# Performance work log

Hardware: AMD Instinct MI355X
Metric: run time of the kernel (lower is better)

The kernel has to match this reference:

```python
import jax, jax.numpy as jnp
import numpy as np

N_NODES = 5000
N_EDGES = 50000
BATCH = 8
SEQ = 12
IN_CH = 2
HID = 64
OUT_CH = 1
K = 3
N_LAYERS = 2


def setup_inputs() -> dict:
    key = jax.random.key(0)
    ks = jax.random.split(key, 20)
    d = {}
    d["x"] = jax.random.normal(ks[0], (BATCH, SEQ, N_NODES, IN_CH), dtype=jnp.float32)
    d["edge_index"] = jax.random.randint(ks[1], (2, N_EDGES), 0, N_NODES, dtype=jnp.int32)

    def w(k, fin):
        return jax.random.normal(k, (2, K, fin, HID), dtype=jnp.float32) * 0.05

    fins = [IN_CH + HID, HID + HID]
    i = 2
    for l in range(N_LAYERS):
        for g in ("z", "r", "h"):
            d["W" + g + str(l)] = w(ks[i], fins[l]); i += 1
            d["b" + g + str(l)] = jnp.zeros((HID,), jnp.float32)
    d["Wo"] = jax.random.normal(ks[i], (HID, OUT_CH), dtype=jnp.float32) * 0.05
    d["bo"] = jnp.zeros((OUT_CH,), jnp.float32)
    return d


def reference(x, edge_index,
              Wz0, bz0, Wr0, br0, Wh0, bh0,
              Wz1, bz1, Wr1, br1, Wh1, bh1,
              Wo, bo):
    B, T, N, _ = x.shape
    src, dst = edge_index[0], edge_index[1]
    ones = jnp.ones(src.shape, x.dtype)
    deg_out = jax.ops.segment_sum(ones, src, num_segments=N)
    deg_in = jax.ops.segment_sum(ones, dst, num_segments=N)
    inv = lambda dgr: jnp.where(dgr > 0, 1.0 / dgr, 0.0)
    norm_out = inv(deg_out)[src]  # [E], 1/deg_out(src)
    norm_in = inv(deg_in)[dst]    # [E], 1/deg_in(dst)

    def prop(X, norm):
        # X: [N, B, F] -> sparse matvec via gather/scatter
        msg = norm[:, None, None] * X[src]
        return jax.ops.segment_sum(msg, dst, num_segments=N)

    def dconv(X, W, b):
        # X: [N, B, Fin]; W: [2, K, Fin, H]; dual-direction Chebyshev diffusion
        H = jnp.einsum('nbf,fh->nbh', X, W[0, 0] + W[1, 0])
        Tx0o = Tx0i = X
        Tx1o = prop(X, norm_out)
        Tx1i = prop(X, norm_in)
        H = H + jnp.einsum('nbf,fh->nbh', Tx1o, W[0, 1]) \
              + jnp.einsum('nbf,fh->nbh', Tx1i, W[1, 1])
        for k in range(2, W.shape[1]):
            Tx2o = 2.0 * prop(Tx1o, norm_out) - Tx0o
            Tx2i = 2.0 * prop(Tx1i, norm_in) - Tx0i
            H = H + jnp.einsum('nbf,fh->nbh', Tx2o, W[0, k]) \
                  + jnp.einsum('nbf,fh->nbh', Tx2i, W[1, k])
            Tx0o, Tx1o = Tx1o, Tx2o
            Tx0i, Tx1i = Tx1i, Tx2i
        return H + b

    def cell(Xin, H, p):
        Wz, bz, Wr, br, Wh, bh = p
        XH = jnp.concatenate([Xin, H], axis=-1)
        Z = jax.nn.sigmoid(dconv(XH, Wz, bz))
        R = jax.nn.sigmoid(dconv(XH, Wr, br))
        Ht = jnp.tanh(dconv(jnp.concatenate([Xin, H * R], axis=-1), Wh, bh))
        return Z * H + (1.0 - Z) * Ht

    layers = [(Wz0, bz0, Wr0, br0, Wh0, bh0), (Wz1, bz1, Wr1, br1, Wh1, bh1)]
    hid = Wo.shape[0]
    h0 = jnp.zeros((len(layers), N, B, hid), x.dtype)
    xs = jnp.transpose(x, (1, 2, 0, 3))  # [T, N, B, F]

    def step(h, xt):
        inp = xt
        new_h = []
        for l, p in enumerate(layers):
            hl = cell(inp, h[l], p)
            new_h.append(hl)
            inp = hl
        h = jnp.stack(new_h)
        out = jnp.einsum('nbh,ho->nbo', h[-1], Wo) + bo
        return h, out

    _, outs = jax.lax.scan(step, h0, xs)      # [T, N, B, O]
    return jnp.transpose(outs, (2, 0, 1, 3))  # [B, T, N, O]
```

## Files before the change

### kernel.cpp

```cpp
#include <hip/hip_runtime.h>
#include <math.h>

#define NNODES 5000
#define NEDGES 50000
#define SEQT 12
#define NB 40000
#define MAXDEG 128

typedef __attribute__((ext_vector_type(8))) _Float16 half8;
typedef __attribute__((ext_vector_type(2))) _Float16 half2v;
typedef __attribute__((ext_vector_type(4))) float f32x4;


__global__ void count_deg_k(const int* __restrict__ ei, int* deg_out, int* deg_in){
    int e = blockIdx.x*blockDim.x + threadIdx.x;
    if (e < NEDGES){
        atomicAdd(&deg_out[ei[e]], 1);
        atomicAdd(&deg_in[ei[NEDGES + e]], 1);
    }
}

__global__ void scan_k(const int* __restrict__ deg_in, int* __restrict__ row_ptr){
    __shared__ int part[256];
    int tid = threadIdx.x;
    int base = tid*20;
    int loc[20]; int s = 0;
    for (int i=0;i<20;i++){
        int idx = base+i;
        int v = (idx < NNODES) ? deg_in[idx] : 0;
        loc[i] = s; s += v;
    }
    part[tid] = s;
    __syncthreads();
    for (int off=1; off<256; off<<=1){
        int v = (tid>=off) ? part[tid-off] : 0;
        __syncthreads();
        part[tid] += v;
        __syncthreads();
    }
    int prev = (tid==0) ? 0 : part[tid-1];
    for (int i=0;i<20;i++){
        int idx = base+i;
        if (idx < NNODES) row_ptr[idx] = prev + loc[i];
    }
    if (tid==255) row_ptr[NNODES] = part[255];
}

__global__ void fill_csr_k(const int* __restrict__ ei, const int* __restrict__ deg_out,
                           const int* __restrict__ deg_in, const int* __restrict__ row_ptr,
                           int* cursor, int* __restrict__ csr_src,
                           float* __restrict__ csr_wo, float* __restrict__ csr_wi){
    int e = blockIdx.x*blockDim.x + threadIdx.x;
    if (e >= NEDGES) return;
    int s = ei[e], d = ei[NEDGES+e];
    int pos = atomicAdd(&cursor[d], 1);
    int slot = row_ptr[d] + pos;
    csr_src[slot] = s;
    csr_wo[slot] = 1.f/(float)deg_out[s];
    csr_wi[slot] = 1.f/(float)deg_in[d];
}

__global__ void prepack_x_k(const float* __restrict__ x, _Float16* __restrict__ Xtph){
    int idx = blockIdx.x*256 + threadIdx.x;
    if (idx >= SEQT*NB*2) return;
    int tt = idx / (NB*2);
    int r2 = idx - tt*(NB*2);
    int row = r2 >> 1, f = r2 & 1;
    int n = row >> 3, b = row & 7;
    Xtph[idx] = (_Float16)x[((size_t)(b*SEQT+tt)*NNODES + n)*2 + f];
}

__device__ __forceinline__ float wfetch(const float* __restrict__ W, int F, int slot, int f, int c){
    const float* p0 = W + ((size_t)0*F + f)*64 + c;
    const float* p1 = W + ((size_t)1*F + f)*64 + c;
    const float* p2 = W + ((size_t)2*F + f)*64 + c;
    const float* p3 = W + ((size_t)3*F + f)*64 + c;
    const float* p4 = W + ((size_t)4*F + f)*64 + c;
    const float* p5 = W + ((size_t)5*F + f)*64 + c;
    switch(slot){
        case 0: return *p0 + *p3 - *p2 - *p5;
        case 1: return *p1;
        case 2: return *p4;
        case 3: return 2.f * *p2;
        default: return 2.f * *p5;
    }
}

__global__ void pack_l0_k(const float* __restrict__ W, _Float16* __restrict__ wh){
    int idx = blockIdx.x*256 + threadIdx.x;
    if (idx >= 4*11*64) return;
    int lane = idx & 63, rest = idx >> 6;
    int ks = rest % 11, cf = rest / 11;
    int col = cf*16 + (lane & 15);
    int kb = ks*32 + ((lane>>4)<<3);
    size_t o = ((size_t)(ks*4 + cf)*64 + lane)*8;
    for (int j=0;j<8;j++){
        int k = kb + j;
        float v = 0.f;
        if (ks == 0){
            if (k < 10) v = wfetch(W, 66, k>>1, k&1, col);
        } else {
            int slot = (ks-1)>>1;
            int f = 2 + k - 32 - 64*slot;
            v = wfetch(W, 66, slot, f, col);
        }
        wh[o+j] = (_Float16)v;
    }
}

__global__ void pack_l1_k(const float* __restrict__ W, _Float16* __restrict__ wh){
    int idx = blockIdx.x*256 + threadIdx.x;
    if (idx >= 4*20*64) return;
    int lane = idx & 63, rest = idx >> 6;
    int ks = rest % 20, cf = rest / 20;
    int col = cf*16 + (lane & 15);
    int kb = ks*32 + ((lane>>4)<<3);
    int slot = ks >> 2;
    size_t o = ((size_t)(ks*4 + cf)*64 + lane)*8;
    for (int j=0;j<8;j++){
        int k = kb + j;
        int f = k - slot*128;
        wh[o+j] = (_Float16)wfetch(W, 128, slot, f, col);
    }
}


__global__ __launch_bounds__(64) void k_f1(int aCount,
    const _Float16* __restrict__ h0h, const _Float16* __restrict__ h1h,
    _Float16* __restrict__ T1o64, _Float16* __restrict__ T1i64,
    const _Float16* __restrict__ Xt,
    _Float16* __restrict__ Th1o, _Float16* __restrict__ Th1i, _Float16* __restrict__ XTh,
    const int* __restrict__ rp, const int* __restrict__ cs,
    const float* __restrict__ cwo, const float* __restrict__ cwi){
    __shared__ int s_o[MAXDEG]; __shared__ float swo[MAXDEG], swi[MAXDEG];
    const int bx = blockIdx.x;
    const bool isA = bx < aCount;
    const int n = isA ? bx : bx - aCount;
    int beg = rp[n], deg = rp[n+1]-beg;
    int nst = deg < MAXDEG ? deg : MAXDEG;
    for (int j=threadIdx.x; j<nst; j+=64){
        s_o[j] = cs[beg+j]*512;
        swo[j] = cwo[beg+j]; swi[j] = cwi[beg+j];
    }
    __syncthreads();
    const _Float16* S = isA ? h1h : h0h;
    _Float16* Yo = isA ? T1o64 : Th1o;
    _Float16* Yi = isA ? T1i64 : Th1i;
    int off = threadIdx.x*8;
    {
        float ao[8] = {0,0,0,0,0,0,0,0}, ai[8] = {0,0,0,0,0,0,0,0};
        for (int j=0;j<nst;j++){
            half8 v = *(const half8*)(S + s_o[j] + off);
            float wo=swo[j], wi=swi[j];
            #pragma unroll
            for (int e=0;e<8;e++){
                float xv = (float)v[e];
                ao[e]=fmaf(wo,xv,ao[e]); ai[e]=fmaf(wi,xv,ai[e]);
            }
        }
        for (int j=nst;j<deg;j++){
            half8 v = *(const half8*)(S + (size_t)cs[beg+j]*512 + off);
            float wo=cwo[beg+j], wi=cwi[beg+j];
            #pragma unroll
            for (int e=0;e<8;e++){
                float xv = (float)v[e];
                ao[e]=fmaf(wo,xv,ao[e]); ai[e]=fmaf(wi,xv,ai[e]);
            }
        }
        half8 po, pi;
        #pragma unroll
        for (int e=0;e<8;e++){ po[e]=(_Float16)ao[e]; pi[e]=(_Float16)ai[e]; }
        *(half8*)(Yo + (size_t)n*512 + off) = po;
        *(half8*)(Yi + (size_t)n*512 + off) = pi;
    }
    if (!isA && threadIdx.x < 8){
        int b = threadIdx.x;
        float ax0=0,ax1=0, ay0=0,ay1=0;
        for (int j=0;j<nst;j++){
            int src = s_o[j] >> 9;
            half2v v = *(const half2v*)(Xt + src*16 + b*2);
            float x0=(float)v[0], x1=(float)v[1];
            ax0=fmaf(swo[j],x0,ax0); ax1=fmaf(swo[j],x1,ax1);
            ay0=fmaf(swi[j],x0,ay0); ay1=fmaf(swi[j],x1,ay1);
        }
        for (int j=nst;j<deg;j++){
            int src = cs[beg+j];
            half2v v = *(const half2v*)(Xt + src*16 + b*2);
            float x0=(float)v[0], x1=(float)v[1];
            ax0=fmaf(cwo[beg+j],x0,ax0); ax1=fmaf(cwo[beg+j],x1,ax1);
            ay0=fmaf(cwi[beg+j],x0,ay0); ay1=fmaf(cwi[beg+j],x1,ay1);
        }
        size_t ro = (size_t)(n*8 + b)*32;
        XTh[ro+0] = Xt[(size_t)(n*8+b)*2+0];
        XTh[ro+1] = Xt[(size_t)(n*8+b)*2+1];
        XTh[ro+2] = (_Float16)ax0; XTh[ro+3] = (_Float16)ax1;
        XTh[ro+4] = (_Float16)ay0; XTh[ro+5] = (_Float16)ay1;
    }
}

__global__ __launch_bounds__(64) void k_f2(int aCount,
    const _Float16* __restrict__ T1o64, const _Float16* __restrict__ T1i64,
    _Float16* __restrict__ U2o64, _Float16* __restrict__ U2i64,
    const _Float16* __restrict__ Th1o, const _Float16* __restrict__ Th1i,
    _Float16* __restrict__ Th2o, _Float16* __restrict__ Th2i, _Float16* __restrict__ XTh,
    const int* __restrict__ rp, const int* __restrict__ cs,
    const float* __restrict__ cwo, const float* __restrict__ cwi){
    __shared__ int s_o[MAXDEG]; __shared__ float s_w[MAXDEG];
    const int bx = blockIdx.x;
    const bool isA = bx < aCount;
    const int idx = isA ? bx : bx - aCount;
    const int n = idx >> 1, sel = idx & 1;
    const float* cw = sel ? cwi : cwo;
    int beg = rp[n], deg = rp[n+1]-beg;
    int nst = deg < MAXDEG ? deg : MAXDEG;
    for (int j=threadIdx.x; j<nst; j+=64){
        s_o[j] = cs[beg+j]*512;
        s_w[j] = cw[beg+j];
    }
    __syncthreads();
    const _Float16* S = isA ? (sel ? T1i64 : T1o64) : (sel ? Th1i : Th1o);
    _Float16* U = isA ? (sel ? U2i64 : U2o64) : (sel ? Th2i : Th2o);
    int off = threadIdx.x*8;
    {
        float a[8] = {0,0,0,0,0,0,0,0};
        for (int j=0;j<nst;j++){
            half8 v = *(const half8*)(S + s_o[j] + off);
            float w=s_w[j];
            #pragma unroll
            for (int e=0;e<8;e++) a[e]=fmaf(w,(float)v[e],a[e]);
        }
        for (int j=nst;j<deg;j++){
            half8 v = *(const half8*)(S + (size_t)cs[beg+j]*512 + off);
            float w=cw[beg+j];
            #pragma unroll
            for (int e=0;e<8;e++) a[e]=fmaf(w,(float)v[e],a[e]);
        }
        half8 p;
        #pragma unroll
        for (int e=0;e<8;e++) p[e]=(_Float16)a[e];
        *(half8*)(U + (size_t)n*512 + off) = p;
    }
    if (!isA && threadIdx.x < 8){
        int b = threadIdx.x;
        int xo = 2 + 2*sel;
        float a0=0,a1=0;
        for (int j=0;j<nst;j++){
            int src = s_o[j] >> 9;
            half2v v = *(const half2v*)(XTh + (size_t)src*256 + b*32 + xo);
            a0=fmaf(s_w[j],(float)v[0],a0); a1=fmaf(s_w[j],(float)v[1],a1);
        }
        for (int j=nst;j<deg;j++){
            int src = cs[beg+j];
            float w = cw[beg+j];
            half2v v = *(const half2v*)(XTh + (size_t)src*256 + b*32 + xo);
            a0=fmaf(w,(float)v[0],a0); a1=fmaf(w,(float)v[1],a1);
        }
        size_t ro = (size_t)(n*8 + b)*32 + 6 + 2*sel;
        XTh[ro+0] = (_Float16)a0; XTh[ro+1] = (_Float16)a1;
    }
}

__global__ __launch_bounds__(64) void k_f4(int aCount,
    const _Float16* __restrict__ SA, _Float16* __restrict__ YoA, _Float16* __restrict__ YiA,
    const _Float16* __restrict__ SB, _Float16* __restrict__ YoB, _Float16* __restrict__ YiB,
    const int* __restrict__ rp, const int* __restrict__ cs,
    const float* __restrict__ cwo, const float* __restrict__ cwi){
    __shared__ int s_o[MAXDEG]; __shared__ float swo[MAXDEG], swi[MAXDEG];
    const int bx = blockIdx.x;
    const bool isA = bx < aCount;
    const int n = isA ? bx : bx - aCount;
    const _Float16* S = isA ? SA : SB;
    _Float16* Yo = isA ? YoA : YoB;
    _Float16* Yi = isA ? YiA : YiB;
    int beg = rp[n], deg = rp[n+1]-beg;
    int nst = deg < MAXDEG ? deg : MAXDEG;
    for (int j=threadIdx.x; j<nst; j+=64){
        s_o[j] = cs[beg+j]*512;
        swo[j] = cwo[beg+j]; swi[j] = cwi[beg+j];
    }
    __syncthreads();
    int off = threadIdx.x*8;
    float ao[8] = {0,0,0,0,0,0,0,0}, ai[8] = {0,0,0,0,0,0,0,0};
    for (int j=0;j<nst;j++){
        half8 v = *(const half8*)(S + s_o[j] + off);
        float wo=swo[j], wi=swi[j];
        #pragma unroll
        for (int e=0;e<8;e++){
            float xv = (float)v[e];
            ao[e]=fmaf(wo,xv,ao[e]); ai[e]=fmaf(wi,xv,ai[e]);
        }
    }
    for (int j=nst;j<deg;j++){
        half8 v = *(const half8*)(S + (size_t)cs[beg+j]*512 + off);
        float wo=cwo[beg+j], wi=cwi[beg+j];
        #pragma unroll
        for (int e=0;e<8;e++){
            float xv = (float)v[e];
            ao[e]=fmaf(wo,xv,ao[e]); ai[e]=fmaf(wi,xv,ai[e]);
        }
    }
    half8 po, pi;
    #pragma unroll
    for (int e=0;e<8;e++){ po[e]=(_Float16)ao[e]; pi[e]=(_Float16)ai[e]; }
    *(half8*)(Yo + (size_t)n*512 + off) = po;
    *(half8*)(Yi + (size_t)n*512 + off) = pi;
}

__global__ __launch_bounds__(64) void k_f5(int aCount,
    const _Float16* __restrict__ T1oA, const _Float16* __restrict__ T1iA,
    _Float16* __restrict__ U2oA, _Float16* __restrict__ U2iA,
    const _Float16* __restrict__ T1oB, const _Float16* __restrict__ T1iB,
    _Float16* __restrict__ U2oB, _Float16* __restrict__ U2iB,
    const int* __restrict__ rp, const int* __restrict__ cs,
    const float* __restrict__ cwo, const float* __restrict__ cwi){
    __shared__ int s_o[MAXDEG]; __shared__ float s_w[MAXDEG];
    const int bx = blockIdx.x;
    const bool isA = bx < aCount;
    const int idx = isA ? bx : bx - aCount;
    const int n = idx >> 1, sel = idx & 1;
    const _Float16* S = isA ? (sel ? T1iA : T1oA) : (sel ? T1iB : T1oB);
    _Float16* U = isA ? (sel ? U2iA : U2oA) : (sel ? U2iB : U2oB);
    const float* cw = sel ? cwi : cwo;
    int beg = rp[n], deg = rp[n+1]-beg;
    int nst = deg < MAXDEG ? deg : MAXDEG;
    for (int j=threadIdx.x; j<nst; j+=64){
        s_o[j] = cs[beg+j]*512;
        s_w[j] = cw[beg+j];
    }
    __syncthreads();
    int off = threadIdx.x*8;
    float a[8] = {0,0,0,0,0,0,0,0};
    for (int j=0;j<nst;j++){
        half8 v = *(const half8*)(S + s_o[j] + off);
        float w=s_w[j];
        #pragma unroll
        for (int e=0;e<8;e++) a[e]=fmaf(w,(float)v[e],a[e]);
    }
    for (int j=nst;j<deg;j++){
        half8 v = *(const half8*)(S + (size_t)cs[beg+j]*512 + off);
        float w=cw[beg+j];
        #pragma unroll
        for (int e=0;e<8;e++) a[e]=fmaf(w,(float)v[e],a[e]);
    }
    half8 p;
    #pragma unroll
    for (int e=0;e<8;e++) p[e]=(_Float16)a[e];
    *(half8*)(U + (size_t)n*512 + off) = p;
}


struct KD { const _Float16* a; int st; };
struct GA { KD kd[20]; };

template<int NK, int NG, int EPI>
__device__ __forceinline__ void gemm_body(char* smemraw, int bxm, const GA& ga,
    const _Float16* __restrict__ wh0, const float* __restrict__ b0,
    const _Float16* __restrict__ wh1, const float* __restrict__ b1,
    float* __restrict__ Z, _Float16* __restrict__ Gout,
    float* __restrict__ Hf, _Float16* __restrict__ Hh,
    const float* __restrict__ Wo, const float* __restrict__ bo,
    float* __restrict__ out, int t){
    _Float16* ldsb = (_Float16*)smemraw;
    float* spr = (float*)(smemraw + (size_t)4*NG*2048);
    const int tid = threadIdx.x;
    const int lane = tid & 63, wv = tid >> 6, rl = lane & 15, kg = lane >> 4;
    const int m0 = bxm*64 + (wv&1)*32;
    const int cfb = (wv>>1)*2;
    const _Float16* wsrc[2] = {wh0, wh1};

    half8 srg[NG];
    half8 a0, a1, a0n, a1n;

    auto sload = [&](int ks){
        #pragma unroll
        for (int j=0;j<NG;j++)
            srg[j] = *(const half8*)(wsrc[j] + (size_t)ks*2048 + tid*8);
    };
    auto swrite = [&](int buf){
        #pragma unroll
        for (int j=0;j<NG;j++)
            *(half8*)&ldsb[buf*(NG*2048) + j*2048 + tid*8] = srg[j];
    };
    auto aload = [&](int ks, half8& x0, half8& x1){
        const _Float16* base = ga.kd[ks].a;
        const int st = ga.kd[ks].st;
        x0 = *(const half8*)(base + (size_t)(m0+rl)*st + kg*8);
        x1 = *(const half8*)(base + (size_t)(m0+16+rl)*st + kg*8);
    };

    f32x4 acc[NG][2][2];
    #pragma unroll
    for (int g=0; g<NG; ++g)
        #pragma unroll
        for (int cc=0; cc<2; ++cc)
            #pragma unroll
            for (int mr=0; mr<2; ++mr){
                acc[g][cc][mr][0]=0.f; acc[g][cc][mr][1]=0.f;
                acc[g][cc][mr][2]=0.f; acc[g][cc][mr][3]=0.f;
            }

    sload(0); swrite(0);
    if (NK>1) sload(1);
    aload(0, a0, a1);
    __syncthreads();
    for (int ks=0; ks<NK; ++ks){
        const int cur = ks & 1;
        if (ks+1 < NK){ swrite(cur^1); aload(ks+1, a0n, a1n); }
        if (ks+2 < NK) sload(ks+2);
        #pragma unroll
        for (int g=0; g<NG; ++g){
            #pragma unroll
            for (int cc=0; cc<2; ++cc){
                half8 bv = *(const half8*)&ldsb[cur*(NG*2048) + g*2048 + (cfb+cc)*512 + lane*8];
                acc[g][cc][0] = __builtin_amdgcn_mfma_f32_16x16x32_f16(a0, bv, acc[g][cc][0], 0, 0, 0);
                acc[g][cc][1] = __builtin_amdgcn_mfma_f32_16x16x32_f16(a1, bv, acc[g][cc][1], 0, 0, 0);
            }
        }
        __syncthreads();
        a0 = a0n; a1 = a1n;
    }

    if constexpr (EPI == 0){
        #pragma unroll
        for (int cc=0; cc<2; ++cc){
            const int col = (cfb+cc)*16 + rl;
            float bzv = b0[col], brv = b1[col];
            #pragma unroll
            for (int mr=0; mr<2; ++mr)
                #pragma unroll
                for (int i=0;i<4;i++){
                    int row = m0 + mr*16 + kg*4 + i;
                    float z = 1.f/(1.f+__expf(-(acc[0][cc][mr][i] + bzv)));
                    float r = 1.f/(1.f+__expf(-(acc[NG-1][cc][mr][i] + brv)));
                    size_t ix = (size_t)row*64 + col;
                    Z[ix] = z;
                    Gout[ix] = (_Float16)(Hf[ix]*r);
                }
        }
    } else {
        float pr[2][4] = {{0.f,0.f,0.f,0.f},{0.f,0.f,0.f,0.f}};
        #pragma unroll
        for (int cc=0; cc<2; ++cc){
            const int col = (cfb+cc)*16 + rl;
            float bv = b0[col];
            float wo_c = 0.f;
            if constexpr (EPI == 2) wo_c = Wo[col];
            #pragma unroll
            for (int mr=0; mr<2; ++mr)
                #pragma unroll
                for (int i=0;i<4;i++){
                    int row = m0 + mr*16 + kg*4 + i;
                    float ht = tanhf(acc[0][cc][mr][i] + bv);
                    size_t ix = (size_t)row*64 + col;
                    float z = Z[ix];
                    float hn = z*Hf[ix] + (1.f-z)*ht;
                    Hf[ix] = hn;
                    Hh[ix] = (_Float16)hn;
                    if constexpr (EPI == 2) pr[mr][i] = fmaf(hn, wo_c, pr[mr][i]);
                }
        }
        if constexpr (EPI == 2){
            #pragma unroll
            for (int mr=0; mr<2; ++mr)
                #pragma unroll
                for (int i=0;i<4;i++){
                    float v = pr[mr][i];
                    v += __shfl_xor(v, 1);
                    v += __shfl_xor(v, 2);
                    v += __shfl_xor(v, 4);
                    v += __shfl_xor(v, 8);
                    if (rl == 0) spr[wv*32 + mr*16 + kg*4 + i] = v;
                }
            __syncthreads();
            if (tid < 64){
                int r = tid;
                float v = spr[(r>>5)*32 + (r&31)] + spr[((r>>5)|2)*32 + (r&31)] + bo[0];
                int row = bxm*64 + r;
                int n = row >> 3, b = row & 7;
                out[(size_t)(b*SEQT + t)*NNODES + n] = v;
            }
        }
    }
}

__global__ __launch_bounds__(256) void k_f3(int aCount,
    GA gaA, const _Float16* whA0, const float* bA0, const _Float16* whA1, const float* bA1,
    float* ZA, _Float16* GoA, float* HfA,
    GA gaB, const _Float16* whB0, const float* bB0, const _Float16* whB1, const float* bB1,
    float* ZB, _Float16* GoB, float* HfB){
    __shared__ __align__(16) char smem[4*2*2048 + 512];
    if (blockIdx.x < aCount)
        gemm_body<20,2,0>(smem, blockIdx.x, gaA, whA0, bA0, whA1, bA1,
                          ZA, GoA, HfA, nullptr, nullptr, nullptr, nullptr, 0);
    else
        gemm_body<11,2,0>(smem, blockIdx.x - aCount, gaB, whB0, bB0, whB1, bB1,
                          ZB, GoB, HfB, nullptr, nullptr, nullptr, nullptr, 0);
}

__global__ __launch_bounds__(256) void k_f6(int aCount,
    GA gaA, const _Float16* whA, const float* bA,
    float* ZA, float* HfA, _Float16* HhA,
    const float* Wo, const float* bo, float* out, int t,
    GA gaB, const _Float16* whB, const float* bB,
    float* ZB, float* HfB, _Float16* HhB){
    __shared__ __align__(16) char smem[4*1*2048 + 512];
    if (blockIdx.x < aCount)
        gemm_body<20,1,2>(smem, blockIdx.x, gaA, whA, bA, nullptr, nullptr,
                          ZA, nullptr, HfA, HhA, Wo, bo, out, t);
    else
        gemm_body<11,1,1>(smem, blockIdx.x - aCount, gaB, whB, bB, nullptr, nullptr,
                          ZB, nullptr, HfB, HhB, nullptr, nullptr, nullptr, 0);
}


extern "C" void kernel_launch(void* const* d_in, const int* in_sizes, int n_in,
                              void* d_out, int out_size, void* d_ws, size_t ws_size,
                              hipStream_t stream){
    (void)in_sizes; (void)n_in; (void)out_size; (void)ws_size;
    const float* x  = (const float*)d_in[0];
    const int*   ei = (const int*)d_in[1];
    const float* Wz[2] = {(const float*)d_in[2],  (const float*)d_in[8]};
    const float* bz[2] = {(const float*)d_in[3],  (const float*)d_in[9]};
    const float* Wr[2] = {(const float*)d_in[4],  (const float*)d_in[10]};
    const float* br[2] = {(const float*)d_in[5],  (const float*)d_in[11]};
    const float* Wh[2] = {(const float*)d_in[6],  (const float*)d_in[12]};
    const float* bh[2] = {(const float*)d_in[7],  (const float*)d_in[13]};
    const float* Wo = (const float*)d_in[14];
    const float* bo = (const float*)d_in[15];
    float* out = (float*)d_out;

    char* p = (char*)d_ws;
    auto alloc = [&](size_t bytes)->char*{
        char* r = p; p += (bytes + 255) & ~(size_t)255; return r;
    };
    const size_t H64  = (size_t)NB*64*2;
    const size_t F64  = (size_t)NB*64*4;

    _Float16* Xtph = (_Float16*)alloc((size_t)SEQT*NB*2*2);
    float*    h0f = (float*)alloc(F64);
    float*    h1f = (float*)alloc(F64);
    float*    Z0  = (float*)alloc(F64);
    float*    Z1  = (float*)alloc(F64);
    _Float16* h0hb[2];
    h0hb[0] = (_Float16*)alloc(H64);
    h0hb[1] = (_Float16*)alloc(H64);
    _Float16* h1h = (_Float16*)alloc(H64);
    _Float16* XTh = (_Float16*)alloc((size_t)NB*32*2);
    _Float16* Th1o = (_Float16*)alloc(H64);
    _Float16* Th1i = (_Float16*)alloc(H64);
    _Float16* Th2o = (_Float16*)alloc(H64);
    _Float16* Th2i = (_Float16*)alloc(H64);
    _Float16* G0L0 = (_Float16*)alloc(H64);
    _Float16* G1o0 = (_Float16*)alloc(H64);
    _Float16* G1i0 = (_Float16*)alloc(H64);
    _Float16* G2o0 = (_Float16*)alloc(H64);
    _Float16* G2i0 = (_Float16*)alloc(H64);
    _Float16* T1o64 = (_Float16*)alloc(H64);
    _Float16* T1i64 = (_Float16*)alloc(H64);
    _Float16* U2o64 = (_Float16*)alloc(H64);
    _Float16* U2i64 = (_Float16*)alloc(H64);
    _Float16* G0p  = (_Float16*)alloc(H64);
    _Float16* G1o1 = (_Float16*)alloc(H64);
    _Float16* G1i1 = (_Float16*)alloc(H64);
    _Float16* G2o1 = (_Float16*)alloc(H64);
    _Float16* G2i1 = (_Float16*)alloc(H64);
    _Float16 *whl0[3], *whl1[3];
    for (int g=0; g<3; ++g){
        whl0[g] = (_Float16*)alloc((size_t)4*11*64*8*2);
        whl1[g] = (_Float16*)alloc((size_t)4*20*64*8*2);
    }
    int* deg_out = (int*)alloc(NNODES*4);
    int* deg_in  = (int*)alloc(NNODES*4);
    int* row_ptr = (int*)alloc((NNODES+1)*4);
    int* cursor  = (int*)alloc(NNODES*4);
    int* csr_src = (int*)alloc(NEDGES*4);
    float* csr_wo = (float*)alloc(NEDGES*4);
    float* csr_wi = (float*)alloc(NEDGES*4);

    hipMemsetAsync(deg_out, 0, NNODES*4, stream);
    hipMemsetAsync(deg_in,  0, NNODES*4, stream);
    hipMemsetAsync(cursor,  0, NNODES*4, stream);
    hipMemsetAsync(h0f, 0, F64, stream);
    hipMemsetAsync(h1f, 0, F64, stream);
    hipMemsetAsync(h0hb[0], 0, H64, stream);
    hipMemsetAsync(h0hb[1], 0, H64, stream);
    hipMemsetAsync(h1h, 0, H64, stream);
    hipMemsetAsync(XTh, 0, (size_t)NB*32*2, stream);

    count_deg_k<<<(NEDGES+255)/256, 256, 0, stream>>>(ei, deg_out, deg_in);
    scan_k<<<1, 256, 0, stream>>>(deg_in, row_ptr);
    fill_csr_k<<<(NEDGES+255)/256, 256, 0, stream>>>(ei, deg_out, deg_in, row_ptr,
                                                     cursor, csr_src, csr_wo, csr_wi);
    prepack_x_k<<<(SEQT*NB*2+255)/256, 256, 0, stream>>>(x, Xtph);
    const float* Wptr0[3] = {Wz[0], Wr[0], Wh[0]};
    const float* Wptr1[3] = {Wz[1], Wr[1], Wh[1]};
    for (int g=0; g<3; ++g){
        pack_l0_k<<<(4*11*64+255)/256, 256, 0, stream>>>(Wptr0[g], whl0[g]);
        pack_l1_k<<<(4*20*64+255)/256, 256, 0, stream>>>(Wptr1[g], whl1[g]);
    }

    GA gaL0zr[2] = {}, gaL1zr[2] = {}, gaL1h[2] = {}, gaL0h = {};
    const _Float16* hsrc[4] = {Th1o, Th1i, Th2o, Th2i};
    const _Float16* g64s[4] = {T1o64, T1i64, U2o64, U2i64};
    for (int pp=0; pp<2; ++pp){
        const _Float16* t64[5] = {h0hb[pp], Th1o, Th1i, Th2o, Th2i};
        gaL0zr[pp].kd[0] = {XTh, 32};
        for (int s=0; s<5; ++s){
            gaL0zr[pp].kd[1+2*s] = {t64[s], 64};
            gaL0zr[pp].kd[2+2*s] = {t64[s]+32, 64};
        }
        gaL1zr[pp].kd[0] = {h0hb[pp], 64};    gaL1zr[pp].kd[1] = {h0hb[pp]+32, 64};
        gaL1zr[pp].kd[2] = {h1h, 64};         gaL1zr[pp].kd[3] = {h1h+32, 64};
        for (int s=0; s<4; ++s){
            gaL1zr[pp].kd[4+4*s+0] = {hsrc[s], 64};
            gaL1zr[pp].kd[4+4*s+1] = {hsrc[s]+32, 64};
            gaL1zr[pp].kd[4+4*s+2] = {g64s[s], 64};
            gaL1zr[pp].kd[4+4*s+3] = {g64s[s]+32, 64};
        }
        gaL1h[pp].kd[0] = {h0hb[pp], 64};  gaL1h[pp].kd[1] = {h0hb[pp]+32, 64};
        gaL1h[pp].kd[2] = {G0p, 64};       gaL1h[pp].kd[3] = {G0p+32, 64};
        const _Float16* gh[4] = {G1o1, G1i1, G2o1, G2i1};
        for (int s=0; s<4; ++s){
            gaL1h[pp].kd[4+4*s+0] = {hsrc[s], 64};
            gaL1h[pp].kd[4+4*s+1] = {hsrc[s]+32, 64};
            gaL1h[pp].kd[4+4*s+2] = {gh[s], 64};
            gaL1h[pp].kd[4+4*s+3] = {gh[s]+32, 64};
        }
    }
    {
        const _Float16* g64[5] = {G0L0, G1o0, G1i0, G2o0, G2i0};
        gaL0h.kd[0] = {XTh, 32};
        for (int s=0; s<5; ++s){
            gaL0h.kd[1+2*s] = {g64[s], 64};
            gaL0h.kd[2+2*s] = {g64[s]+32, 64};
        }
    }

    k_f1<<<NNODES, 64, 0, stream>>>(0, h0hb[1], h1h, T1o64, T1i64,
        Xtph, Th1o, Th1i, XTh, row_ptr, csr_src, csr_wo, csr_wi);
    k_f2<<<2*NNODES, 64, 0, stream>>>(0, T1o64, T1i64, U2o64, U2i64,
        Th1o, Th1i, Th2o, Th2i, XTh, row_ptr, csr_src, csr_wo, csr_wi);
    k_f3<<<625, 256, 0, stream>>>(0,
        gaL1zr[1], whl1[0], bz[1], whl1[1], br[1], Z1, G0p, h1f,
        gaL0zr[1], whl0[0], bz[0], whl0[1], br[0], Z0, G0L0, h0f);
    k_f4<<<NNODES, 64, 0, stream>>>(0, G0p, G1o1, G1i1, G0L0, G1o0, G1i0,
        row_ptr, csr_src, csr_wo, csr_wi);
    k_f5<<<2*NNODES, 64, 0, stream>>>(0, G1o1, G1i1, G2o1, G2i1,
        G1o0, G1i0, G2o0, G2i0, row_ptr, csr_src, csr_wo, csr_wi);
    k_f6<<<625, 256, 0, stream>>>(0,
        gaL1h[1], whl1[2], bh[1], Z1, h1f, h1h, Wo, bo, out, 0,
        gaL0h, whl0[2], bh[0], Z0, h0f, h0hb[0]);

    for (int s=0; s<SEQT; ++s){
        const int pr = s & 1;
        const int doB = (s+1 < SEQT) ? 1 : 0;
        const _Float16* xp = Xtph + (size_t)(doB ? s+1 : s)*NB*2;
        k_f1<<<2*NNODES, 64, 0, stream>>>(NNODES,
            h0hb[pr], h1h, T1o64, T1i64, xp, Th1o, Th1i, XTh,
            row_ptr, csr_src, csr_wo, csr_wi);
        k_f2<<<4*NNODES, 64, 0, stream>>>(2*NNODES,
            T1o64, T1i64, U2o64, U2i64,
            Th1o, Th1i, Th2o, Th2i, XTh, row_ptr, csr_src, csr_wo, csr_wi);
        k_f3<<<625*(1+doB), 256, 0, stream>>>(625,
            gaL1zr[pr], whl1[0], bz[1], whl1[1], br[1], Z1, G0p, h1f,
            gaL0zr[pr], whl0[0], bz[0], whl0[1], br[0], Z0, G0L0, h0f);
        k_f4<<<NNODES*(1+doB), 64, 0, stream>>>(NNODES,
            G0p, G1o1, G1i1, G0L0, G1o0, G1i0, row_ptr, csr_src, csr_wo, csr_wi);
        k_f5<<<2*NNODES*(1+doB), 64, 0, stream>>>(2*NNODES,
            G1o1, G1i1, G2o1, G2i1, G1o0, G1i0, G2o0, G2i0,
            row_ptr, csr_src, csr_wo, csr_wi);
        k_f6<<<625*(1+doB), 256, 0, stream>>>(625,
            gaL1h[pr], whl1[2], bh[1], Z1, h1f, h1h, Wo, bo, out, s,
            gaL0h, whl0[2], bh[0], Z0, h0f, h0hb[(s+1)&1]);
    }
}
```

Before: 1.947 ms.

## Read GEMM weights directly from global memory instead of staging through LDS

Drops the double-buffered LDS staging of the weight tiles and the per-k-step block barriers in the fused GRU gate GEMMs. Each wave now loads its B fragments straight from global memory, which should stay cache resident, and the k loop is fully unrolled so the compiler can schedule loads ahead of the MFMAs. This removes the barrier and LDS traffic and the LDS footprint. In exchange it gives up explicit software prefetch, and every wave issues its own global weight loads.

```diff
diff --git a/kernel.cpp b/kernel.cpp
--- a/kernel.cpp
+++ b/kernel.cpp
@@ -353,40 +353,17 @@
 struct GA { KD kd[20]; };
 
 template<int NK, int NG, int EPI>
-__device__ __forceinline__ void gemm_body(char* smemraw, int bxm, const GA& ga,
+__device__ __forceinline__ void gemm_body(float* spr, int bxm, const GA& ga,
     const _Float16* __restrict__ wh0, const float* __restrict__ b0,
     const _Float16* __restrict__ wh1, const float* __restrict__ b1,
     float* __restrict__ Z, _Float16* __restrict__ Gout,
     float* __restrict__ Hf, _Float16* __restrict__ Hh,
     const float* __restrict__ Wo, const float* __restrict__ bo,
     float* __restrict__ out, int t){
-    _Float16* ldsb = (_Float16*)smemraw;
-    float* spr = (float*)(smemraw + (size_t)4*NG*2048);
     const int tid = threadIdx.x;
     const int lane = tid & 63, wv = tid >> 6, rl = lane & 15, kg = lane >> 4;
     const int m0 = bxm*64 + (wv&1)*32;
     const int cfb = (wv>>1)*2;
-    const _Float16* wsrc[2] = {wh0, wh1};
-
-    half8 srg[NG];
-    half8 a0, a1, a0n, a1n;
-
-    auto sload = [&](int ks){
-        #pragma unroll
-        for (int j=0;j<NG;j++)
-            srg[j] = *(const half8*)(wsrc[j] + (size_t)ks*2048 + tid*8);
-    };
-    auto swrite = [&](int buf){
-        #pragma unroll
-        for (int j=0;j<NG;j++)
-            *(half8*)&ldsb[buf*(NG*2048) + j*2048 + tid*8] = srg[j];
-    };
-    auto aload = [&](int ks, half8& x0, half8& x1){
-        const _Float16* base = ga.kd[ks].a;
-        const int st = ga.kd[ks].st;
-        x0 = *(const half8*)(base + (size_t)(m0+rl)*st + kg*8);
-        x1 = *(const half8*)(base + (size_t)(m0+16+rl)*st + kg*8);
-    };
 
     f32x4 acc[NG][2][2];
     #pragma unroll
@@ -399,25 +376,22 @@
                 acc[g][cc][mr][2]=0.f; acc[g][cc][mr][3]=0.f;
             }
 
-    sload(0); swrite(0);
-    if (NK>1) sload(1);
-    aload(0, a0, a1);
-    __syncthreads();
+    #pragma unroll
     for (int ks=0; ks<NK; ++ks){
-        const int cur = ks & 1;
-        if (ks+1 < NK){ swrite(cur^1); aload(ks+1, a0n, a1n); }
-        if (ks+2 < NK) sload(ks+2);
+        const _Float16* base = ga.kd[ks].a;
+        const int st = ga.kd[ks].st;
+        half8 a0 = *(const half8*)(base + (size_t)(m0+rl)*st + kg*8);
+        half8 a1 = *(const half8*)(base + (size_t)(m0+16+rl)*st + kg*8);
         #pragma unroll
         for (int g=0; g<NG; ++g){
+            const _Float16* ws = g ? wh1 : wh0;
             #pragma unroll
             for (int cc=0; cc<2; ++cc){
-                half8 bv = *(const half8*)&ldsb[cur*(NG*2048) + g*2048 + (cfb+cc)*512 + lane*8];
+                half8 bv = *(const half8*)(ws + (size_t)ks*2048 + (cfb+cc)*512 + lane*8);
                 acc[g][cc][0] = __builtin_amdgcn_mfma_f32_16x16x32_f16(a0, bv, acc[g][cc][0], 0, 0, 0);
                 acc[g][cc][1] = __builtin_amdgcn_mfma_f32_16x16x32_f16(a1, bv, acc[g][cc][1], 0, 0, 0);
             }
         }
-        __syncthreads();
-        a0 = a0n; a1 = a1n;
     }
 
     if constexpr (EPI == 0){
@@ -488,12 +462,11 @@
     float* ZA, _Float16* GoA, float* HfA,
     GA gaB, const _Float16* whB0, const float* bB0, const _Float16* whB1, const float* bB1,
     float* ZB, _Float16* GoB, float* HfB){
-    __shared__ __align__(16) char smem[4*2*2048 + 512];
     if (blockIdx.x < aCount)
-        gemm_body<20,2,0>(smem, blockIdx.x, gaA, whA0, bA0, whA1, bA1,
+        gemm_body<20,2,0>(nullptr, blockIdx.x, gaA, whA0, bA0, whA1, bA1,
                           ZA, GoA, HfA, nullptr, nullptr, nullptr, nullptr, 0);
     else
-        gemm_body<11,2,0>(smem, blockIdx.x - aCount, gaB, whB0, bB0, whB1, bB1,
+        gemm_body<11,2,0>(nullptr, blockIdx.x - aCount, gaB, whB0, bB0, whB1, bB1,
                           ZB, GoB, HfB, nullptr, nullptr, nullptr, nullptr, 0);
 }
 
@@ -503,12 +476,12 @@
     const float* Wo, const float* bo, float* out, int t,
     GA gaB, const _Float16* whB, const float* bB,
     float* ZB, float* HfB, _Float16* HhB){
-    __shared__ __align__(16) char smem[4*1*2048 + 512];
+    __shared__ float spr[128];
     if (blockIdx.x < aCount)
-        gemm_body<20,1,2>(smem, blockIdx.x, gaA, whA, bA, nullptr, nullptr,
+        gemm_body<20,1,2>(spr, blockIdx.x, gaA, whA, bA, nullptr, nullptr,
                           ZA, nullptr, HfA, HhA, Wo, bo, out, t);
     else
-        gemm_body<11,1,1>(smem, blockIdx.x - aCount, gaB, whB, bB, nullptr, nullptr,
+        gemm_body<11,1,1>(spr, blockIdx.x - aCount, gaB, whB, bB, nullptr, nullptr,
                           ZB, nullptr, HfB, HhB, nullptr, nullptr, nullptr, 0);
 }
 
```

New measurement: 2.010 ms. 1.03x slower.
